# Kernel optimization log

Hardware: AMD Instinct MI355X
Metric: run time of the kernel (lower is better)

Reference implementation:

```python
import jax, jax.numpy as jnp
import numpy as np

B, S, F, D, H, L, FF, M, NH, D2, O = 4, 1024, 20, 512, 8, 4, 2048, 32, 3, 256, 1
HD = D // H


def ln(x, g, b, eps=1e-5):
    m = jnp.mean(x, -1, keepdims=True)
    v = jnp.mean((x - m) ** 2, -1, keepdims=True)
    return (x - m) / jnp.sqrt(v + eps) * g + b


def posenc(seq_len, d_model):
    pos = jnp.arange(seq_len, dtype=jnp.float32)[:, None]
    div = jnp.exp(jnp.arange(0, d_model, 2, dtype=jnp.float32) * (-np.log(10000.0) / d_model))
    pe = jnp.zeros((seq_len, d_model), jnp.float32)
    pe = pe.at[:, 0::2].set(jnp.sin(pos * div)).at[:, 1::2].set(jnp.cos(pos * div))
    return pe


def setup_inputs():
    key = jax.random.key(0)
    ks = iter(jax.random.split(key, 64))
    g = lambda shape, s=0.02: jax.random.normal(next(ks), shape, jnp.float32) * s
    z = lambda shape: jnp.zeros(shape, jnp.float32)
    o = lambda shape: jnp.ones(shape, jnp.float32)
    return {
        'x': jax.random.normal(next(ks), (B, S, F), jnp.float32),
        'in_W': g((F, D)), 'in_b': z((D,)), 'in_ln_g': o((D,)), 'in_ln_b': z((D,)),
        'ln1_g': o((L, D)), 'ln1_b': z((L, D)),
        'Wq': g((L, D, D)), 'bq': z((L, D)), 'Wk': g((L, D, D)), 'bk': z((L, D)),
        'Wv': g((L, D, D)), 'bv': z((L, D)), 'Wo': g((L, D, D)), 'bo': z((L, D)),
        'rel': g((L, 2 * M + 1, HD)),
        'ln2_g': o((L, D)), 'ln2_b': z((L, D)),
        'W1': g((L, D, FF)), 'b1': z((L, FF)), 'W2': g((L, FF, D)), 'b2': z((L, D)),
        'gWq': g((D, D)), 'gbq': z((D,)), 'gWk': g((D, D)), 'gbk': z((D,)),
        'gWv': g((D, D)), 'gbv': z((D,)), 'gWo': g((D, D)), 'gbo': z((D,)),
        'hW1': g((NH, D, D2)), 'hb1': z((NH, D2)), 'hln_g': o((NH, D2)), 'hln_b': z((NH, D2)),
        'hW2': g((NH, D2, O)), 'hb2': z((NH, O)),
    }


def _heads(xx, Wq, bq, Wk, bk, Wv, bv):
    # project and split into heads -> [B,H,S,HD]
    q = (xx @ Wq + bq).reshape(B, S, H, HD).transpose(0, 2, 1, 3)
    k = (xx @ Wk + bk).reshape(B, S, H, HD).transpose(0, 2, 1, 3)
    v = (xx @ Wv + bv).reshape(B, S, H, HD).transpose(0, 2, 1, 3)
    return q, k, v


def _block(x, l1g, l1b, Wq, bq, Wk, bk, Wv, bv, Wo, bo, rel, l2g, l2b, W1, b1, W2, b2):
    xn = ln(x, l1g, l1b)
    q, k, v = _heads(xn, Wq, bq, Wk, bk, Wv, bv)
    scores = jnp.einsum('bhqd,bhkd->bhqk', q, k) / jnp.sqrt(jnp.float32(HD))
    pos = jnp.arange(S)
    rel_idx = jnp.clip(pos[None, :] - pos[:, None], -M, M) + M  # [S,S]
    rel_enc = rel[rel_idx]  # [S,S,HD]
    # relative-position bias (NOT scaled by sqrt(HD), matching the torch code)
    scores = scores + jnp.einsum('bhqd,qkd->bhqk', q, rel_enc)
    w = jax.nn.softmax(scores, axis=-1)
    out = jnp.einsum('bhqk,bhkd->bhqd', w, v).transpose(0, 2, 1, 3).reshape(B, S, D)
    x = x + out @ Wo + bo
    xn = ln(x, l2g, l2b)
    ff = jax.nn.gelu(xn @ W1 + b1, approximate=False) @ W2 + b2
    return x + ff


def _forward(x, in_W, in_b, in_ln_g, in_ln_b, ln1_g, ln1_b, Wq, bq, Wk, bk, Wv, bv, Wo, bo, rel,
             ln2_g, ln2_b, W1, b1, W2, b2, gWq, gbq, gWk, gbk, gWv, gbv, gWo, gbo,
             hW1, hb1, hln_g, hln_b, hW2, hb2):
    h = ln(x @ in_W + in_b, in_ln_g, in_ln_b)
    h = h + posenc(S, D)[None]
    for l in range(L):
        h = _block(h, ln1_g[l], ln1_b[l], Wq[l], bq[l], Wk[l], bk[l], Wv[l], bv[l],
                   Wo[l], bo[l], rel[l], ln2_g[l], ln2_b[l], W1[l], b1[l], W2[l], b2[l])
    # global multi-head self-attention (standard scaled dot-product)
    q, k, v = _heads(h, gWq, gbq, gWk, gbk, gWv, gbv)
    w = jax.nn.softmax(jnp.einsum('bhqd,bhkd->bhqk', q, k) / jnp.sqrt(jnp.float32(HD)), axis=-1)
    go = jnp.einsum('bhqk,bhkd->bhqd', w, v).transpose(0, 2, 1, 3).reshape(B, S, D) @ gWo + gbo
    ctx = go[:, -1, :]  # last-timestep context [B,D]
    y = jnp.einsum('bd,hde->bhe', ctx, hW1) + hb1  # [B,NH,D2]
    y = jax.nn.relu(ln(y, hln_g, hln_b))
    return jnp.einsum('bhe,heo->bho', y, hW2) + hb2  # [B,NH,O]


def reference(x, in_W, in_b, in_ln_g, in_ln_b, ln1_g, ln1_b, Wq, bq, Wk, bk, Wv, bv, Wo, bo, rel,
              ln2_g, ln2_b, W1, b1, W2, b2, gWq, gbq, gWk, gbk, gWv, gbv, gWo, gbo,
              hW1, hb1, hln_g, hln_b, hW2, hb2):
    return _forward(x, in_W, in_b, in_ln_g, in_ln_b, ln1_g, ln1_b, Wq, bq, Wk, bk, Wv, bv, Wo, bo,
                    rel, ln2_g, ln2_b, W1, b1, W2, b2, gWq, gbq, gWk, gbk, gWv, gbv, gWo, gbo,
                    hW1, hb1, hln_g, hln_b, hW2, hb2)
```

## Files before the change

kernel.cpp:

```cpp
#include <hip/hip_runtime.h>
#include <math.h>

#define DEV __device__ __forceinline__

constexpr int BSD = 4 * 1024 * 512;

typedef __attribute__((ext_vector_type(8))) short bf16x8;
typedef __attribute__((ext_vector_type(4))) float f32x4;

typedef __attribute__((address_space(1))) const void global_cvoid;
typedef __attribute__((address_space(3))) void lds_void;

DEV ushort f2b(float f) {
  union { float f; uint u; } x{f};
  uint r = x.u + 0x7fff + ((x.u >> 16) & 1);
  return (ushort)(r >> 16);
}
DEV float b2f(ushort u) {
  union { uint u; float f; } x{(uint)u << 16};
  return x.f;
}
DEV int swz128(int b) { return b ^ (((b >> 7) & 7) << 4); }

DEV float wave_sum(float v) {
#pragma unroll
  for (int m = 32; m >= 1; m >>= 1) v += __shfl_xor(v, m, 64);
  return v;
}
DEV float wave_max(float v) {
#pragma unroll
  for (int m = 32; m >= 1; m >>= 1) v = fmaxf(v, __shfl_xor(v, m, 64));
  return v;
}
DEV float block_sum(float v, float* sm) {
  v = wave_sum(v);
  __syncthreads();
  if ((threadIdx.x & 63) == 0) sm[threadIdx.x >> 6] = v;
  __syncthreads();
  return sm[0] + sm[1] + sm[2] + sm[3];
}
DEV float block_max(float v, float* sm) {
  v = wave_max(v);
  __syncthreads();
  if ((threadIdx.x & 63) == 0) sm[threadIdx.x >> 6] = v;
  __syncthreads();
  return fmaxf(fmaxf(sm[0], sm[1]), fmaxf(sm[2], sm[3]));
}

__global__ __launch_bounds__(256) void k_inproj(
    const float* __restrict__ x, const float* __restrict__ W,
    const float* __restrict__ bias, const float* __restrict__ g,
    const float* __restrict__ bt, float* __restrict__ h) {
  int r = blockIdx.x;
  int s = r & 1023;
  int t = threadIdx.x;
  __shared__ float xr[20];
  __shared__ float red[4];
  if (t < 20) xr[t] = x[r * 20 + t];
  __syncthreads();
  float o0 = bias[t], o1 = bias[t + 256];
#pragma unroll
  for (int f = 0; f < 20; f++) {
    float xv = xr[f];
    o0 += xv * W[f * 512 + t];
    o1 += xv * W[f * 512 + t + 256];
  }
  float mean = block_sum(o0 + o1, red) * (1.f / 512.f);
  float d0 = o0 - mean, d1 = o1 - mean;
  float var = block_sum(d0 * d0 + d1 * d1, red) * (1.f / 512.f);
  float rs = rsqrtf(var + 1e-5f);
  float n0 = d0 * rs * g[t] + bt[t];
  float n1 = d1 * rs * g[t + 256] + bt[t + 256];
  const float c1 = -9.210340371976184f / 512.f;
  {
    int c = t;
    float div = __expf((float)(c & ~1) * c1);
    float arg = (float)s * div;
    n0 += (c & 1) ? __cosf(arg) : __sinf(arg);
  }
  {
    int c = t + 256;
    float div = __expf((float)(c & ~1) * c1);
    float arg = (float)s * div;
    n1 += (c & 1) ? __cosf(arg) : __sinf(arg);
  }
  float* hr = h + (size_t)r * 512;
  hr[t] = n0;
  hr[t + 256] = n1;
}

__global__ __launch_bounds__(256) void k_lnw(
    const float* __restrict__ x, const float* __restrict__ g,
    const float* __restrict__ bt, ushort* __restrict__ y) {
  int lane = threadIdx.x & 63;
  int r = blockIdx.x * 4 + (threadIdx.x >> 6);
  const float4* xr = (const float4*)(x + (size_t)r * 512);
  float4 a = xr[lane];
  float4 c = xr[lane + 64];
  float s = a.x + a.y + a.z + a.w + c.x + c.y + c.z + c.w;
  float mean = wave_sum(s) * (1.f / 512.f);
  float d0 = a.x - mean, d1 = a.y - mean, d2 = a.z - mean, d3 = a.w - mean;
  float e0 = c.x - mean, e1 = c.y - mean, e2 = c.z - mean, e3 = c.w - mean;
  float vs = d0 * d0 + d1 * d1 + d2 * d2 + d3 * d3 +
             e0 * e0 + e1 * e1 + e2 * e2 + e3 * e3;
  float var = wave_sum(vs) * (1.f / 512.f);
  float rs = rsqrtf(var + 1e-5f);
  const float4* g4 = (const float4*)g;
  const float4* b4 = (const float4*)bt;
  float4 g0 = g4[lane], g1 = g4[lane + 64];
  float4 b0 = b4[lane], b1 = b4[lane + 64];
  ushort4 o0 = {f2b(d0 * rs * g0.x + b0.x), f2b(d1 * rs * g0.y + b0.y),
                f2b(d2 * rs * g0.z + b0.z), f2b(d3 * rs * g0.w + b0.w)};
  ushort4 o1 = {f2b(e0 * rs * g1.x + b1.x), f2b(e1 * rs * g1.y + b1.y),
                f2b(e2 * rs * g1.z + b1.z), f2b(e3 * rs * g1.w + b1.w)};
  ushort4* yr = (ushort4*)(y + (size_t)r * 512);
  yr[lane] = o0;
  yr[lane + 64] = o1;
}

struct PJobs {
  const float* s[19];
  ushort* d[19];
};
__global__ __launch_bounds__(256) void k_wprep(PJobs j, int K, int N) {
  const float* src = j.s[blockIdx.z];
  ushort* dst = j.d[blockIdx.z];
  __shared__ float ld[32][33];
  int n0 = blockIdx.x * 32, k0 = blockIdx.y * 32;
  int c = threadIdx.x & 31, r0 = threadIdx.x >> 5;
#pragma unroll
  for (int i = 0; i < 4; i++)
    ld[r0 + i * 8][c] = src[(size_t)(k0 + r0 + i * 8) * N + n0 + c];
  __syncthreads();
#pragma unroll
  for (int i = 0; i < 4; i++)
    dst[(size_t)(n0 + r0 + i * 8) * K + k0 + c] = f2b(ld[c][r0 + i * 8]);
}

__global__ __launch_bounds__(256) void k_relprep(const float* __restrict__ rel,
                                                 ushort* __restrict__ relb) {
  int i = blockIdx.x * 256 + threadIdx.x;
  int l = blockIdx.y;
  int r = i >> 6, d = i & 63;
  float v = (r < 65) ? rel[((size_t)l * 65 + r) * 64 + d] * 8.f : 0.f;
  relb[(size_t)l * 80 * 64 + i] = f2b(v);
}

template <int BM, int BN, int MODE, int FUSEB>
__global__ __launch_bounds__(256) void k_mg(
    const ushort* __restrict__ A, const ushort* __restrict__ Bt,
    const float* __restrict__ bias0, const float* __restrict__ bias1,
    const float* __restrict__ bias2, void* __restrict__ Cv,
    ushort* __restrict__ C2, int K, int ldc, int gx) {
  __shared__ __align__(16) ushort As[2][BM * 64];
  __shared__ __align__(16) ushort Bs[2][BN * 64];
  int nwg = gridDim.x;
  int id = blockIdx.x;
  int logical = (id & 7) * (nwg >> 3) + (id >> 3);
  int bx = logical % gx, by = logical / gx;
  int row0 = by * BM, col0 = bx * BN;
  int t = threadIdx.x, lane = t & 63, w = t >> 6;
  int rl15 = lane & 15, l16 = lane >> 4;
  constexpr int WR = (BM == 128 && BN == 128) ? 2 : BM / 32;
  constexpr int WC = 4 / WR;
  constexpr int MI = BM / (WR * 16);
  constexpr int NI = BN / (WC * 16);
  int wr = w % WR, wc = w / WR;
  int wrow = wr * MI * 16;
  int wcol = wc * NI * 16;
  f32x4 acc[MI][NI] = {};

  auto stage = [&](int buf, int kb) {
#pragma unroll
    for (int i = 0; i < BM / 32; i++) {
      int blk = w * (BM / 32) + i;
      int lb = blk * 1024 + lane * 16;
      int lg = swz128(lb);
      int r = lg >> 7, cb = (lg & 127) >> 1;
      __builtin_amdgcn_global_load_lds(
          (global_cvoid*)(A + (size_t)(row0 + r) * K + kb + cb),
          (lds_void*)((char*)As[buf] + blk * 1024), 16, 0, 0);
    }
#pragma unroll
    for (int i = 0; i < BN / 32; i++) {
      int blk = w * (BN / 32) + i;
      int lb = blk * 1024 + lane * 16;
      int lg = swz128(lb);
      int r = lg >> 7, cb = (lg & 127) >> 1;
      __builtin_amdgcn_global_load_lds(
          (global_cvoid*)(Bt + (size_t)(col0 + r) * K + kb + cb),
          (lds_void*)((char*)Bs[buf] + blk * 1024), 16, 0, 0);
    }
  };

  stage(0, 0);
  __syncthreads();
  int nkt = K >> 6;
  for (int kt = 0; kt < nkt; kt++) {
    int cur = kt & 1;
    if (kt + 1 < nkt) stage(cur ^ 1, (kt + 1) << 6);
#pragma unroll
    for (int ks = 0; ks < 2; ks++) {
      bf16x8 af[MI], bfr[NI];
#pragma unroll
      for (int mi = 0; mi < MI; mi++) {
        int row = wrow + mi * 16 + rl15;
        af[mi] =
            *(const bf16x8*)((char*)As[cur] + swz128(row * 128 + ks * 64 + l16 * 16));
      }
#pragma unroll
      for (int ni = 0; ni < NI; ni++) {
        int row = wcol + ni * 16 + rl15;
        bfr[ni] =
            *(const bf16x8*)((char*)Bs[cur] + swz128(row * 128 + ks * 64 + l16 * 16));
      }
#pragma unroll
      for (int mi = 0; mi < MI; mi++)
#pragma unroll
        for (int ni = 0; ni < NI; ni++)
          acc[mi][ni] = __builtin_amdgcn_mfma_f32_16x16x32_bf16(af[mi], bfr[ni],
                                                                acc[mi][ni], 0, 0, 0);
    }
    __syncthreads();
  }
#pragma unroll
  for (int mi = 0; mi < MI; mi++) {
#pragma unroll
    for (int ni = 0; ni < NI; ni++) {
      int col = col0 + wcol + ni * 16 + rl15;
      float bv;
      if (FUSEB == 1) {
        const float* bp = bias0;
        int c = col;
        if (c >= 1024) { bp = bias2; c -= 1024; }
        else if (c >= 512) { bp = bias1; c -= 512; }
        bv = bp[c];
      } else if (FUSEB == 2) {
        bv = (col < 512) ? bias0[col] : bias1[col - 512];
      } else {
        bv = bias0[col];
      }
#pragma unroll
      for (int r = 0; r < 4; r++) {
        int row = row0 + wrow + mi * 16 + l16 * 4 + r;
        float val = acc[mi][ni][r] + bv;
        if (FUSEB == 1 && col < 512) val *= 0.125f;
        if (MODE == 0) {
          ushort bval = f2b(val);
          if (FUSEB == 1 && col >= 1024) {
            int dg = col - 1024;
            int bh = (row >> 10) * 8 + (dg >> 6);
            C2[((size_t)bh * 64 + (dg & 63)) * 1024 + (row & 1023)] = bval;
          } else {
            ((ushort*)Cv)[(size_t)row * ldc + col] = bval;
          }
        } else if (MODE == 1) {
          float* Cp = (float*)Cv + (size_t)row * ldc + col;
          *Cp = *Cp + val;
        } else if (MODE == 2) {
          val = 0.5f * val * (1.f + erff(val * 0.70710678118654752f));
          ((ushort*)Cv)[(size_t)row * ldc + col] = f2b(val);
        } else {
          float* Cp = (float*)Cv + (size_t)row * ldc + col;
          float nv = *Cp + val;
          *Cp = nv;
          C2[(size_t)row * ldc + col] = f2b(nv);
        }
      }
    }
  }
}

__global__ __launch_bounds__(256) void k_attn3(
    const ushort* __restrict__ qkv, const ushort* __restrict__ vT,
    const ushort* __restrict__ relb, ushort* __restrict__ ao) {
  __shared__ __align__(16) ushort Ks[2][64 * 64];
  __shared__ __align__(16) ushort Vts[2][64 * 64];
  __shared__ ushort qrlb[4][16][66];
  __shared__ __align__(16) ushort Pl[4][16 * 72];
  int t = threadIdx.x, lane = t & 63, w = t >> 6;
  int bid = blockIdx.x;
  int p = bid & 31;
  int h = p & 7, b = p >> 3;
  int q0 = (bid >> 5) * 64;
  int qw = q0 + w * 16;
  int rl15 = lane & 15, l16 = lane >> 4;
  size_t baseq = ((size_t)b * 1024) * 1536 + h * 64;
  size_t basek = baseq + 512;
  const ushort* vTb = vT + ((size_t)(b * 8 + h)) * 64 * 1024;

  bf16x8 aq[2];
#pragma unroll
  for (int ks = 0; ks < 2; ks++)
    aq[ks] = *(const bf16x8*)(qkv + baseq + (size_t)(qw + rl15) * 1536 + ks * 32 + l16 * 8);

#pragma unroll
  for (int nb = 0; nb < 5; nb++) {
    f32x4 rc = {};
#pragma unroll
    for (int ks = 0; ks < 2; ks++) {
      bf16x8 rb =
          *(const bf16x8*)(relb + (size_t)(nb * 16 + rl15) * 64 + ks * 32 + l16 * 8);
      rc = __builtin_amdgcn_mfma_f32_16x16x32_bf16(aq[ks], rb, rc, 0, 0, 0);
    }
    int col = nb * 16 + rl15;
    if (col < 65) {
#pragma unroll
      for (int r = 0; r < 4; r++) qrlb[w][l16 * 4 + r][col] = f2b(rc[r]);
    }
  }

  auto stage = [&](int buf, int kb) {
#pragma unroll
    for (int i = 0; i < 2; i++) {
      int blk = w * 2 + i;
      int lb = blk * 1024 + lane * 16;
      int lg = swz128(lb);
      int r = lg >> 7, cb = (lg & 127) >> 1;
      __builtin_amdgcn_global_load_lds(
          (global_cvoid*)(qkv + basek + (size_t)(kb + r) * 1536 + cb),
          (lds_void*)((char*)Ks[buf] + blk * 1024), 16, 0, 0);
      __builtin_amdgcn_global_load_lds(
          (global_cvoid*)(vTb + (size_t)r * 1024 + kb + cb),
          (lds_void*)((char*)Vts[buf] + blk * 1024), 16, 0, 0);
    }
  };

  float m_own = -1e30f, l_own = 0.f;
  f32x4 oacc[4] = {};

  stage(0, 0);
  __syncthreads();

  for (int kt = 0; kt < 16; kt++) {
    int kb = kt << 6;
    int cur = kt & 1;
    if (kt < 15) stage(cur ^ 1, kb + 64);

    f32x4 sacc[4] = {};
#pragma unroll
    for (int ks = 0; ks < 2; ks++) {
#pragma unroll
      for (int nb = 0; nb < 4; nb++) {
        bf16x8 kf = *(const bf16x8*)((char*)Ks[cur] +
                                     swz128((nb * 16 + rl15) * 128 + ks * 64 + l16 * 16));
        sacc[nb] = __builtin_amdgcn_mfma_f32_16x16x32_bf16(kf, aq[ks], sacc[nb], 0, 0, 0);
      }
    }

    float sv[4][4];
    bool hiU = (kb >= qw + 47);
    bool loU = (kb + 95 <= qw);
    if (hiU || loU) {
      float crow = b2f(qrlb[w][rl15][hiU ? 64 : 0]);
#pragma unroll
      for (int nb = 0; nb < 4; nb++)
#pragma unroll
        for (int r = 0; r < 4; r++) sv[nb][r] = sacc[nb][r] + crow;
    } else {
      int qg = qw + rl15;
#pragma unroll
      for (int nb = 0; nb < 4; nb++)
#pragma unroll
        for (int r = 0; r < 4; r++) {
          int delta = kb + nb * 16 + l16 * 4 + r - qg;
          delta = delta < -32 ? -32 : (delta > 32 ? 32 : delta);
          sv[nb][r] = sacc[nb][r] + b2f(qrlb[w][rl15][delta + 32]);
        }
    }

    float rowm = sv[0][0];
#pragma unroll
    for (int nb = 0; nb < 4; nb++)
#pragma unroll
      for (int r = 0; r < 4; r++) rowm = fmaxf(rowm, sv[nb][r]);
    rowm = fmaxf(rowm, __shfl_xor(rowm, 16, 64));
    rowm = fmaxf(rowm, __shfl_xor(rowm, 32, 64));

    if (__any(rowm > m_own + 8.f)) {
      float mn = fmaxf(m_own, rowm);
      float sc = __expf(m_own - mn);
      m_own = mn;
      l_own *= sc;
      float s0 = __shfl(sc, l16 * 4 + 0, 64);
      float s1 = __shfl(sc, l16 * 4 + 1, 64);
      float s2 = __shfl(sc, l16 * 4 + 2, 64);
      float s3 = __shfl(sc, l16 * 4 + 3, 64);
#pragma unroll
      for (int nb = 0; nb < 4; nb++) {
        oacc[nb][0] *= s0;
        oacc[nb][1] *= s1;
        oacc[nb][2] *= s2;
        oacc[nb][3] *= s3;
      }
    }

    float pv[4][4];
    float ls = 0.f;
#pragma unroll
    for (int nb = 0; nb < 4; nb++)
#pragma unroll
      for (int r = 0; r < 4; r++) {
        float e = __expf(sv[nb][r] - m_own);
        pv[nb][r] = e;
        ls += e;
      }
    ls += __shfl_xor(ls, 16, 64);
    ls += __shfl_xor(ls, 32, 64);
    l_own += ls;

#pragma unroll
    for (int nb = 0; nb < 4; nb++) {
      uint w0 = (uint)f2b(pv[nb][0]) | ((uint)f2b(pv[nb][1]) << 16);
      uint w1 = (uint)f2b(pv[nb][2]) | ((uint)f2b(pv[nb][3]) << 16);
      uint* dst = (uint*)&Pl[w][rl15 * 72 + nb * 16 + l16 * 4];
      dst[0] = w0;
      dst[1] = w1;
    }
#pragma unroll
    for (int ks = 0; ks < 2; ks++) {
      bf16x8 pa = *(const bf16x8*)&Pl[w][rl15 * 72 + ks * 32 + l16 * 8];
#pragma unroll
      for (int nb = 0; nb < 4; nb++) {
        bf16x8 bv8 = *(const bf16x8*)((char*)Vts[cur] +
                                      swz128((nb * 16 + rl15) * 128 + ks * 64 + l16 * 16));
        oacc[nb] = __builtin_amdgcn_mfma_f32_16x16x32_bf16(pa, bv8, oacc[nb], 0, 0, 0);
      }
    }
    __syncthreads();
  }

  float linv[4];
#pragma unroll
  for (int r = 0; r < 4; r++) linv[r] = 1.f / __shfl(l_own, l16 * 4 + r, 64);
  size_t baseo = ((size_t)b * 1024) * 512 + h * 64;
#pragma unroll
  for (int nb = 0; nb < 4; nb++) {
    int d = nb * 16 + rl15;
#pragma unroll
    for (int r = 0; r < 4; r++) {
      int row = q0 + w * 16 + l16 * 4 + r;
      ao[baseo + (size_t)row * 512 + d] = f2b(oacc[nb][r] * linv[r]);
    }
  }
}

__global__ __launch_bounds__(256) void k_gattn2(
    const ushort* __restrict__ xn, const float* __restrict__ gWq,
    const float* __restrict__ gbq, const ushort* __restrict__ kv,
    float* __restrict__ ctxa) {
  int t = threadIdx.x;
  int h = blockIdx.x & 7, b = blockIdx.x >> 3;
  __shared__ float Qs[64];
  __shared__ float qp[4][64];
  __shared__ float sc[1024];
  __shared__ float red[4];
  __shared__ float op[4][64];
  {
    int d = t & 63, q = t >> 6;
    const ushort* xr = xn + (size_t)(b * 1024 + 1023) * 512;
    float acc = 0.f;
    for (int k = q * 128; k < q * 128 + 128; k++)
      acc += b2f(xr[k]) * gWq[(size_t)k * 512 + h * 64 + d];
    qp[q][d] = acc;
  }
  __syncthreads();
  if (t < 64)
    Qs[t] = (qp[0][t] + qp[1][t] + qp[2][t] + qp[3][t] + gbq[h * 64 + t]) * 0.125f;
  __syncthreads();
  float lm = -1e30f;
  float sv[4];
#pragma unroll
  for (int jj = 0; jj < 4; jj++) {
    int j = t + (jj << 8);
    const bf16x8* kp = (const bf16x8*)(kv + (size_t)(b * 1024 + j) * 1024 + h * 64);
    float s = 0.f;
#pragma unroll
    for (int c = 0; c < 8; c++) {
      bf16x8 v8 = kp[c];
#pragma unroll
      for (int e = 0; e < 8; e++) s += Qs[c * 8 + e] * b2f((ushort)v8[e]);
    }
    sv[jj] = s;
    lm = fmaxf(lm, s);
  }
  float bm = block_max(lm, red);
  float ls = 0.f;
#pragma unroll
  for (int jj = 0; jj < 4; jj++) {
    float e = __expf(sv[jj] - bm);
    sc[t + (jj << 8)] = e;
    ls += e;
  }
  float bs = block_sum(ls, red);
  int d = t & 63, qd = t >> 6;
  float acc = 0.f;
  for (int j = qd << 8; j < (qd << 8) + 256; j++)
    acc += sc[j] * b2f(kv[(size_t)(b * 1024 + j) * 1024 + 512 + h * 64 + d]);
  op[qd][d] = acc;
  __syncthreads();
  if (t < 64) {
    float r = (op[0][t] + op[1][t] + op[2][t] + op[3][t]) / bs;
    ctxa[b * 512 + h * 64 + t] = r;
  }
}

__global__ __launch_bounds__(256) void k_rowgemm(
    const float* __restrict__ xrow, const float* __restrict__ W,
    const float* __restrict__ bias, float* __restrict__ y) {
  int b = blockIdx.x >> 4;
  int col0 = (blockIdx.x & 15) * 32;
  int t = threadIdx.x;
  int col = t & 31, kq = t >> 5;
  __shared__ float xs[512];
  __shared__ float part[8][32];
  if (t < 128) ((float4*)xs)[t] = ((const float4*)(xrow + b * 512))[t];
  __syncthreads();
  float acc = 0.f;
  const float* Wp = W + (size_t)(kq * 64) * 512 + col0 + col;
#pragma unroll 8
  for (int k = 0; k < 64; k++) acc += xs[kq * 64 + k] * Wp[(size_t)k * 512];
  part[kq][col] = acc;
  __syncthreads();
  if (t < 32) {
    float s = part[0][t] + part[1][t] + part[2][t] + part[3][t] +
              part[4][t] + part[5][t] + part[6][t] + part[7][t];
    y[b * 512 + col0 + t] = s + bias[col0 + t];
  }
}

__global__ __launch_bounds__(512) void k_head(
    const float* __restrict__ ctx, const float* __restrict__ hW1,
    const float* __restrict__ hb1, const float* __restrict__ hg,
    const float* __restrict__ hbt, const float* __restrict__ hW2,
    const float* __restrict__ hb2, float* __restrict__ out) {
  int b = blockIdx.x / 3, nh = blockIdx.x % 3;
  int t = threadIdx.x;
  __shared__ float cs[512];
  __shared__ float part[2][256];
  __shared__ float red[8];
  if (t < 128) ((float4*)cs)[t] = ((const float4*)(ctx + b * 512))[t];
  __syncthreads();
  {
    int col = t & 255, kh = t >> 8;
    float acc = 0.f;
    const float* Wp = hW1 + ((size_t)nh * 512 + kh * 256) * 256 + col;
#pragma unroll 8
    for (int d = 0; d < 256; d++) acc += cs[kh * 256 + d] * Wp[(size_t)d * 256];
    part[kh][col] = acc;
  }
  __syncthreads();
  float y = 0.f;
  if (t < 256) y = part[0][t] + part[1][t] + hb1[nh * 256 + t];
  float v = wave_sum(t < 256 ? y : 0.f);
  if ((t & 63) == 0) red[t >> 6] = v;
  __syncthreads();
  float mean = (red[0] + red[1] + red[2] + red[3] + red[4] + red[5] + red[6] +
                red[7]) * (1.f / 256.f);
  float dv = (t < 256) ? (y - mean) : 0.f;
  float v2 = wave_sum(dv * dv);
  __syncthreads();
  if ((t & 63) == 0) red[t >> 6] = v2;
  __syncthreads();
  float var = (red[0] + red[1] + red[2] + red[3] + red[4] + red[5] + red[6] +
               red[7]) * (1.f / 256.f);
  float rs = rsqrtf(var + 1e-5f);
  float yn = 0.f;
  if (t < 256) {
    yn = dv * rs * hg[nh * 256 + t] + hbt[nh * 256 + t];
    yn = fmaxf(yn, 0.f) * hW2[nh * 256 + t];
  }
  float v3 = wave_sum(yn);
  __syncthreads();
  if ((t & 63) == 0) red[t >> 6] = v3;
  __syncthreads();
  if (t == 0) {
    float s = red[0] + red[1] + red[2] + red[3] + red[4] + red[5] + red[6] + red[7];
    out[b * 3 + nh] = s + hb2[nh];
  }
}

extern "C" void kernel_launch(void* const* d_in, const int* in_sizes, int n_in,
                              void* d_out, int out_size, void* d_ws, size_t ws_size,
                              hipStream_t stream) {
  const float* x = (const float*)d_in[0];
  const float* in_W = (const float*)d_in[1];
  const float* in_b = (const float*)d_in[2];
  const float* in_lng = (const float*)d_in[3];
  const float* in_lnb = (const float*)d_in[4];
  const float* ln1_g = (const float*)d_in[5];
  const float* ln1_b = (const float*)d_in[6];
  const float* Wq = (const float*)d_in[7];
  const float* bq = (const float*)d_in[8];
  const float* Wk = (const float*)d_in[9];
  const float* bk = (const float*)d_in[10];
  const float* Wv = (const float*)d_in[11];
  const float* bv = (const float*)d_in[12];
  const float* Wo = (const float*)d_in[13];
  const float* bo = (const float*)d_in[14];
  const float* rel = (const float*)d_in[15];
  const float* ln2_g = (const float*)d_in[16];
  const float* ln2_b = (const float*)d_in[17];
  const float* W1 = (const float*)d_in[18];
  const float* b1 = (const float*)d_in[19];
  const float* W2 = (const float*)d_in[20];
  const float* b2 = (const float*)d_in[21];
  const float* gWq = (const float*)d_in[22];
  const float* gbq = (const float*)d_in[23];
  const float* gWk = (const float*)d_in[24];
  const float* gbk = (const float*)d_in[25];
  const float* gWv = (const float*)d_in[26];
  const float* gbv = (const float*)d_in[27];
  const float* gWo = (const float*)d_in[28];
  const float* gbo = (const float*)d_in[29];
  const float* hW1 = (const float*)d_in[30];
  const float* hb1 = (const float*)d_in[31];
  const float* hlng = (const float*)d_in[32];
  const float* hlnb = (const float*)d_in[33];
  const float* hW2 = (const float*)d_in[34];
  const float* hb2 = (const float*)d_in[35];
  float* out = (float*)d_out;

  uint8_t* wsb = (uint8_t*)d_ws;
  const size_t MB = 1024 * 1024;
  float* h = (float*)(wsb + 0);
  ushort* xn = (ushort*)(wsb + 8 * MB);
  ushort* qkvb = (ushort*)(wsb + 12 * MB);
  ushort* kvb = qkvb;
  ushort* aob = (ushort*)(wsb + 24 * MB);
  ushort* ffb = (ushort*)(wsb + 28 * MB);
  ushort* vTb = ffb;
  ushort* wqkv = (ushort*)(wsb + 44 * MB);
  ushort* wto = (ushort*)(wsb + 50 * MB);
  ushort* wt1 = (ushort*)(wsb + 52 * MB);
  ushort* wt2 = (ushort*)(wsb + 60 * MB);
  ushort* gwkv = (ushort*)(wsb + 68 * MB);
  ushort* relb = (ushort*)(wsb + 70 * MB);
  float* attnlast = (float*)(wsb + 71 * MB);
  float* ctx = attnlast + 4096;

  const size_t W55 = 512 * 512;

  {
    PJobs j{};
    for (int l = 0; l < 4; l++) {
      j.s[l * 4 + 0] = Wq + (size_t)l * W55;
      j.d[l * 4 + 0] = wqkv + (size_t)l * 1536 * 512;
      j.s[l * 4 + 1] = Wk + (size_t)l * W55;
      j.d[l * 4 + 1] = wqkv + (size_t)l * 1536 * 512 + 512 * 512;
      j.s[l * 4 + 2] = Wv + (size_t)l * W55;
      j.d[l * 4 + 2] = wqkv + (size_t)l * 1536 * 512 + 1024 * 512;
      j.s[l * 4 + 3] = Wo + (size_t)l * W55;
      j.d[l * 4 + 3] = wto + (size_t)l * W55;
    }
    j.s[16] = gWk; j.d[16] = gwkv;
    j.s[17] = gWv; j.d[17] = gwkv + 512 * 512;
    k_wprep<<<dim3(16, 16, 18), 256, 0, stream>>>(j, 512, 512);
  }
  {
    PJobs j{};
    for (int l = 0; l < 4; l++) {
      j.s[l] = W1 + (size_t)l * 512 * 2048;
      j.d[l] = wt1 + (size_t)l * 2048 * 512;
    }
    k_wprep<<<dim3(64, 16, 4), 256, 0, stream>>>(j, 512, 2048);
  }
  {
    PJobs j{};
    for (int l = 0; l < 4; l++) {
      j.s[l] = W2 + (size_t)l * 2048 * 512;
      j.d[l] = wt2 + (size_t)l * 512 * 2048;
    }
    k_wprep<<<dim3(16, 64, 4), 256, 0, stream>>>(j, 2048, 512);
  }
  k_relprep<<<dim3(20, 4), 256, 0, stream>>>(rel, relb);
  k_inproj<<<4096, 256, 0, stream>>>(x, in_W, in_b, in_lng, in_lnb, h);

  for (int l = 0; l < 4; l++) {
    size_t vo = (size_t)l * 512;
    k_lnw<<<1024, 256, 0, stream>>>(h, ln1_g + vo, ln1_b + vo, xn);
    k_mg<128, 64, 0, 1><<<768, 256, 0, stream>>>(xn, wqkv + (size_t)l * 1536 * 512,
                                                 bq + vo, bk + vo, bv + vo, qkvb,
                                                 vTb, 512, 1536, 24);
    k_attn3<<<512, 256, 0, stream>>>(qkvb, vTb, relb + (size_t)l * 80 * 64, aob);
    k_mg<64, 64, 1, 0><<<512, 256, 0, stream>>>(aob, wto + (size_t)l * W55, bo + vo,
                                                nullptr, nullptr, h, nullptr, 512, 512, 8);
    k_lnw<<<1024, 256, 0, stream>>>(h, ln2_g + vo, ln2_b + vo, xn);
    k_mg<128, 128, 2, 0><<<512, 256, 0, stream>>>(xn, wt1 + (size_t)l * 2048 * 512,
                                                  b1 + (size_t)l * 2048, nullptr, nullptr,
                                                  ffb, nullptr, 512, 2048, 16);
    if (l < 3)
      k_mg<64, 64, 1, 0><<<512, 256, 0, stream>>>(ffb, wt2 + (size_t)l * 512 * 2048,
                                                  b2 + vo, nullptr, nullptr, h, nullptr,
                                                  2048, 512, 8);
    else
      k_mg<64, 64, 3, 0><<<512, 256, 0, stream>>>(ffb, wt2 + (size_t)l * 512 * 2048,
                                                  b2 + vo, nullptr, nullptr, h, xn,
                                                  2048, 512, 8);
  }

  k_mg<128, 64, 0, 2><<<512, 256, 0, stream>>>(xn, gwkv, gbk, gbv, nullptr, kvb,
                                               nullptr, 512, 1024, 16);
  k_gattn2<<<32, 256, 0, stream>>>(xn, gWq, gbq, kvb, attnlast);
  k_rowgemm<<<64, 256, 0, stream>>>(attnlast, gWo, gbo, ctx);
  k_head<<<12, 512, 0, stream>>>(ctx, hW1, hb1, hlng, hlnb, hW2, hb2, out);
}
```

Measured before the change: 516.6 us.

## Split attention key range across two wave groups and merge softmax partials

The attention kernel now runs 512 threads per block. Two groups of four waves each process half of the key sequence, and their partial outputs and max/sum statistics are merged through shared memory at the end. V fragments are read directly from global memory into registers instead of being staged through LDS. The input projection kernel is also rewritten to do one row per wave with wave-level reductions, which removes block-level syncs. The split doubles in-flight parallelism per query tile, at the cost of a final merge step and uncached global V loads.

Result: slower. 565.8 us (+9.5%).

```diff
diff --git a/kernel.cpp b/kernel.cpp
--- a/kernel.cpp
+++ b/kernel.cpp
@@ -51,42 +51,43 @@
     const float* __restrict__ x, const float* __restrict__ W,
     const float* __restrict__ bias, const float* __restrict__ g,
     const float* __restrict__ bt, float* __restrict__ h) {
-  int r = blockIdx.x;
+  int lane = threadIdx.x & 63;
+  int r = blockIdx.x * 4 + (threadIdx.x >> 6);
   int s = r & 1023;
-  int t = threadIdx.x;
-  __shared__ float xr[20];
-  __shared__ float red[4];
-  if (t < 20) xr[t] = x[r * 20 + t];
-  __syncthreads();
-  float o0 = bias[t], o1 = bias[t + 256];
-#pragma unroll
-  for (int f = 0; f < 20; f++) {
-    float xv = xr[f];
-    o0 += xv * W[f * 512 + t];
-    o1 += xv * W[f * 512 + t + 256];
-  }
-  float mean = block_sum(o0 + o1, red) * (1.f / 512.f);
-  float d0 = o0 - mean, d1 = o1 - mean;
-  float var = block_sum(d0 * d0 + d1 * d1, red) * (1.f / 512.f);
+  float xr[20];
+#pragma unroll
+  for (int f = 0; f < 20; f++) xr[f] = x[r * 20 + f];
+  float o[8];
+#pragma unroll
+  for (int j = 0; j < 8; j++) {
+    int c = lane + 64 * j;
+    float acc = bias[c];
+#pragma unroll
+    for (int f = 0; f < 20; f++) acc += xr[f] * W[f * 512 + c];
+    o[j] = acc;
+  }
+  float ssum = 0.f;
+#pragma unroll
+  for (int j = 0; j < 8; j++) ssum += o[j];
+  float mean = wave_sum(ssum) * (1.f / 512.f);
+  float vs = 0.f;
+#pragma unroll
+  for (int j = 0; j < 8; j++) {
+    o[j] -= mean;
+    vs += o[j] * o[j];
+  }
+  float var = wave_sum(vs) * (1.f / 512.f);
   float rs = rsqrtf(var + 1e-5f);
-  float n0 = d0 * rs * g[t] + bt[t];
-  float n1 = d1 * rs * g[t + 256] + bt[t + 256];
   const float c1 = -9.210340371976184f / 512.f;
-  {
-    int c = t;
+#pragma unroll
+  for (int j = 0; j < 8; j++) {
+    int c = lane + 64 * j;
+    float n = o[j] * rs * g[c] + bt[c];
     float div = __expf((float)(c & ~1) * c1);
     float arg = (float)s * div;
-    n0 += (c & 1) ? __cosf(arg) : __sinf(arg);
-  }
-  {
-    int c = t + 256;
-    float div = __expf((float)(c & ~1) * c1);
-    float arg = (float)s * div;
-    n1 += (c & 1) ? __cosf(arg) : __sinf(arg);
-  }
-  float* hr = h + (size_t)r * 512;
-  hr[t] = n0;
-  hr[t + 256] = n1;
+    n += (c & 1) ? __cosf(arg) : __sinf(arg);
+    h[(size_t)r * 512 + c] = n;
+  }
 }
 
 __global__ __launch_bounds__(256) void k_lnw(
@@ -271,19 +272,21 @@
   }
 }
 
-__global__ __launch_bounds__(256) void k_attn3(
+__global__ __launch_bounds__(512, 4) void k_attn4(
     const ushort* __restrict__ qkv, const ushort* __restrict__ vT,
     const ushort* __restrict__ relb, ushort* __restrict__ ao) {
-  __shared__ __align__(16) ushort Ks[2][64 * 64];
-  __shared__ __align__(16) ushort Vts[2][64 * 64];
+  __shared__ __align__(16) ushort Ks[2][2][64 * 64];
   __shared__ ushort qrlb[4][16][66];
-  __shared__ __align__(16) ushort Pl[4][16 * 72];
+  __shared__ __align__(16) ushort Pl[8][16 * 72];
+  __shared__ float Om[4][16][64];
+  __shared__ float Ml[4][16][2];
   int t = threadIdx.x, lane = t & 63, w = t >> 6;
+  int wq = w & 3, kh = w >> 2;
   int bid = blockIdx.x;
   int p = bid & 31;
   int h = p & 7, b = p >> 3;
   int q0 = (bid >> 5) * 64;
-  int qw = q0 + w * 16;
+  int qw = q0 + wq * 16;
   int rl15 = lane & 15, l16 = lane >> 4;
   size_t baseq = ((size_t)b * 1024) * 1536 + h * 64;
   size_t basek = baseq + 512;
@@ -294,55 +297,62 @@
   for (int ks = 0; ks < 2; ks++)
     aq[ks] = *(const bf16x8*)(qkv + baseq + (size_t)(qw + rl15) * 1536 + ks * 32 + l16 * 8);
 
-#pragma unroll
-  for (int nb = 0; nb < 5; nb++) {
-    f32x4 rc = {};
-#pragma unroll
-    for (int ks = 0; ks < 2; ks++) {
-      bf16x8 rb =
-          *(const bf16x8*)(relb + (size_t)(nb * 16 + rl15) * 64 + ks * 32 + l16 * 8);
-      rc = __builtin_amdgcn_mfma_f32_16x16x32_bf16(aq[ks], rb, rc, 0, 0, 0);
-    }
-    int col = nb * 16 + rl15;
-    if (col < 65) {
-#pragma unroll
-      for (int r = 0; r < 4; r++) qrlb[w][l16 * 4 + r][col] = f2b(rc[r]);
-    }
-  }
-
-  auto stage = [&](int buf, int kb) {
+  if (kh == 0) {
+#pragma unroll
+    for (int nb = 0; nb < 5; nb++) {
+      f32x4 rc = {};
+#pragma unroll
+      for (int ks = 0; ks < 2; ks++) {
+        bf16x8 rb =
+            *(const bf16x8*)(relb + (size_t)(nb * 16 + rl15) * 64 + ks * 32 + l16 * 8);
+        rc = __builtin_amdgcn_mfma_f32_16x16x32_bf16(aq[ks], rb, rc, 0, 0, 0);
+      }
+      int col = nb * 16 + rl15;
+      if (col < 65) {
+#pragma unroll
+        for (int r = 0; r < 4; r++) qrlb[wq][l16 * 4 + r][col] = f2b(rc[r]);
+      }
+    }
+  }
+
+  auto stageK = [&](int buf, int kb) {
 #pragma unroll
     for (int i = 0; i < 2; i++) {
-      int blk = w * 2 + i;
+      int blk = wq * 2 + i;
       int lb = blk * 1024 + lane * 16;
       int lg = swz128(lb);
       int r = lg >> 7, cb = (lg & 127) >> 1;
       __builtin_amdgcn_global_load_lds(
           (global_cvoid*)(qkv + basek + (size_t)(kb + r) * 1536 + cb),
-          (lds_void*)((char*)Ks[buf] + blk * 1024), 16, 0, 0);
-      __builtin_amdgcn_global_load_lds(
-          (global_cvoid*)(vTb + (size_t)r * 1024 + kb + cb),
-          (lds_void*)((char*)Vts[buf] + blk * 1024), 16, 0, 0);
+          (lds_void*)((char*)Ks[kh][buf] + blk * 1024), 16, 0, 0);
     }
   };
 
   float m_own = -1e30f, l_own = 0.f;
   f32x4 oacc[4] = {};
 
-  stage(0, 0);
-  __syncthreads();
-
-  for (int kt = 0; kt < 16; kt++) {
-    int kb = kt << 6;
+  stageK(0, kh << 9);
+  __syncthreads();
+
+  for (int kt = 0; kt < 8; kt++) {
+    int kb = (kh << 9) + (kt << 6);
     int cur = kt & 1;
-    if (kt < 15) stage(cur ^ 1, kb + 64);
+    if (kt < 7) stageK(cur ^ 1, kb + 64);
+
+    bf16x8 vf[2][4];
+#pragma unroll
+    for (int ks = 0; ks < 2; ks++)
+#pragma unroll
+      for (int nb = 0; nb < 4; nb++)
+        vf[ks][nb] = *(const bf16x8*)(vTb + (size_t)(nb * 16 + rl15) * 1024 + kb +
+                                      ks * 32 + l16 * 8);
 
     f32x4 sacc[4] = {};
 #pragma unroll
     for (int ks = 0; ks < 2; ks++) {
 #pragma unroll
       for (int nb = 0; nb < 4; nb++) {
-        bf16x8 kf = *(const bf16x8*)((char*)Ks[cur] +
+        bf16x8 kf = *(const bf16x8*)((char*)Ks[kh][cur] +
                                      swz128((nb * 16 + rl15) * 128 + ks * 64 + l16 * 16));
         sacc[nb] = __builtin_amdgcn_mfma_f32_16x16x32_bf16(kf, aq[ks], sacc[nb], 0, 0, 0);
       }
@@ -352,7 +362,7 @@
     bool hiU = (kb >= qw + 47);
     bool loU = (kb + 95 <= qw);
     if (hiU || loU) {
-      float crow = b2f(qrlb[w][rl15][hiU ? 64 : 0]);
+      float crow = b2f(qrlb[wq][rl15][hiU ? 64 : 0]);
 #pragma unroll
       for (int nb = 0; nb < 4; nb++)
 #pragma unroll
@@ -365,7 +375,7 @@
         for (int r = 0; r < 4; r++) {
           int delta = kb + nb * 16 + l16 * 4 + r - qg;
           delta = delta < -32 ? -32 : (delta > 32 ? 32 : delta);
-          sv[nb][r] = sacc[nb][r] + b2f(qrlb[w][rl15][delta + 32]);
+          sv[nb][r] = sacc[nb][r] + b2f(qrlb[wq][rl15][delta + 32]);
         }
     }
 
@@ -421,26 +431,40 @@
     for (int ks = 0; ks < 2; ks++) {
       bf16x8 pa = *(const bf16x8*)&Pl[w][rl15 * 72 + ks * 32 + l16 * 8];
 #pragma unroll
+      for (int nb = 0; nb < 4; nb++)
+        oacc[nb] = __builtin_amdgcn_mfma_f32_16x16x32_bf16(pa, vf[ks][nb],
+                                                           oacc[nb], 0, 0, 0);
+    }
+    __syncthreads();
+  }
+
+  if (kh == 1) {
+#pragma unroll
+    for (int nb = 0; nb < 4; nb++)
+#pragma unroll
+      for (int r = 0; r < 4; r++) Om[wq][l16 * 4 + r][nb * 16 + rl15] = oacc[nb][r];
+    if (l16 == 0) {
+      Ml[wq][rl15][0] = m_own;
+      Ml[wq][rl15][1] = l_own;
+    }
+  }
+  __syncthreads();
+  if (kh == 0) {
+    size_t baseo = ((size_t)b * 1024) * 512 + h * 64;
+#pragma unroll
+    for (int r = 0; r < 4; r++) {
+      int row = l16 * 4 + r;
+      float m1 = __shfl(m_own, row, 64);
+      float l1 = __shfl(l_own, row, 64);
+      float m2 = Ml[wq][row][0], l2 = Ml[wq][row][1];
+      float mn = fmaxf(m1, m2);
+      float s1 = __expf(m1 - mn), s2 = __expf(m2 - mn);
+      float linv = 1.f / (l1 * s1 + l2 * s2);
+#pragma unroll
       for (int nb = 0; nb < 4; nb++) {
-        bf16x8 bv8 = *(const bf16x8*)((char*)Vts[cur] +
-                                      swz128((nb * 16 + rl15) * 128 + ks * 64 + l16 * 16));
-        oacc[nb] = __builtin_amdgcn_mfma_f32_16x16x32_bf16(pa, bv8, oacc[nb], 0, 0, 0);
-      }
-    }
-    __syncthreads();
-  }
-
-  float linv[4];
-#pragma unroll
-  for (int r = 0; r < 4; r++) linv[r] = 1.f / __shfl(l_own, l16 * 4 + r, 64);
-  size_t baseo = ((size_t)b * 1024) * 512 + h * 64;
-#pragma unroll
-  for (int nb = 0; nb < 4; nb++) {
-    int d = nb * 16 + rl15;
-#pragma unroll
-    for (int r = 0; r < 4; r++) {
-      int row = q0 + w * 16 + l16 * 4 + r;
-      ao[baseo + (size_t)row * 512 + d] = f2b(oacc[nb][r] * linv[r]);
+        float val = (oacc[nb][r] * s1 + Om[wq][row][nb * 16 + rl15] * s2) * linv;
+        ao[baseo + (size_t)(qw + row) * 512 + nb * 16 + rl15] = f2b(val);
+      }
     }
   }
 }
@@ -674,7 +698,7 @@
     k_wprep<<<dim3(16, 64, 4), 256, 0, stream>>>(j, 2048, 512);
   }
   k_relprep<<<dim3(20, 4), 256, 0, stream>>>(rel, relb);
-  k_inproj<<<4096, 256, 0, stream>>>(x, in_W, in_b, in_lng, in_lnb, h);
+  k_inproj<<<1024, 256, 0, stream>>>(x, in_W, in_b, in_lng, in_lnb, h);
 
   for (int l = 0; l < 4; l++) {
     size_t vo = (size_t)l * 512;
@@ -682,7 +706,7 @@
     k_mg<128, 64, 0, 1><<<768, 256, 0, stream>>>(xn, wqkv + (size_t)l * 1536 * 512,
                                                  bq + vo, bk + vo, bv + vo, qkvb,
                                                  vTb, 512, 1536, 24);
-    k_attn3<<<512, 256, 0, stream>>>(qkvb, vTb, relb + (size_t)l * 80 * 64, aob);
+    k_attn4<<<512, 512, 0, stream>>>(qkvb, vTb, relb + (size_t)l * 80 * 64, aob);
     k_mg<64, 64, 1, 0><<<512, 256, 0, stream>>>(aob, wto + (size_t)l * W55, bo + vo,
                                                 nullptr, nullptr, h, nullptr, 512, 512, 8);
     k_lnw<<<1024, 256, 0, stream>>>(h, ln2_g + vo, ln2_b + vo, xn);
```
